# Kernel tuning notes

Hardware: AMD Instinct MI355X
Metric: run time of the kernel (lower is better)

The kernel has to match this reference:

```python
import jax, jax.numpy as jnp
import numpy as np

N_NODES = 100000
N_EDGES = 1600000
F_IN = 256
F_HID = 128
BN_EPS = 1e-3


def setup_inputs() -> dict:
    key = jax.random.key(0)
    ks = jax.random.split(key, 10)
    x = jax.random.normal(ks[0], (N_NODES, F_IN), dtype=jnp.float32)
    edge_index = jax.random.randint(ks[1], (2, N_EDGES), 0, N_NODES, dtype=jnp.int64)
    edge_weight = jax.random.uniform(ks[2], (N_EDGES,), dtype=jnp.float32)
    # Layer 0: GCNConv 256 -> 128, Layer 1: GCNConv 128 -> 128
    W0 = jax.random.normal(ks[3], (F_IN, F_HID), dtype=jnp.float32) * (1.0 / np.sqrt(F_IN))
    b0 = jnp.zeros((F_HID,), dtype=jnp.float32)
    g0 = jnp.ones((F_HID,), dtype=jnp.float32)
    beta0 = jnp.zeros((F_HID,), dtype=jnp.float32)
    W1 = jax.random.normal(ks[4], (F_HID, F_HID), dtype=jnp.float32) * (1.0 / np.sqrt(F_HID))
    b1 = jnp.zeros((F_HID,), dtype=jnp.float32)
    g1 = jnp.ones((F_HID,), dtype=jnp.float32)
    beta1 = jnp.zeros((F_HID,), dtype=jnp.float32)
    return {"x": x, "edge_index": edge_index, "edge_weight": edge_weight,
            "W0": W0, "b0": b0, "g0": g0, "beta0": beta0,
            "W1": W1, "b1": b1, "g1": g1, "beta1": beta1}


def _gcn_conv(x, src, dst, ew, W, b):
    # PyG GCNConv: add self-loops (weight 1), symmetric normalization,
    # linear transform, scatter-aggregate over destination, then bias.
    h = x @ W                                            # [N, F_out]
    deg = jax.ops.segment_sum(ew, dst, num_segments=N_NODES) + 1.0  # +1 self-loop
    dinv = jnp.where(deg > 0, jax.lax.rsqrt(deg), 0.0)   # deg^{-1/2}
    norm = dinv[src] * ew * dinv[dst]                    # [E]
    agg = jax.ops.segment_sum(h[src] * norm[:, None], dst, num_segments=N_NODES)
    agg = agg + (dinv * dinv)[:, None] * h               # self-loop contribution
    return agg + b


def _batchnorm(x, gamma, beta):
    # training-mode BatchNorm1d math (batch stats, biased variance), eps=1e-3
    mu = jnp.mean(x, axis=0)
    var = jnp.mean(jnp.square(x - mu), axis=0)
    return (x - mu) * jax.lax.rsqrt(var + BN_EPS) * gamma + beta


def reference(x, edge_index, edge_weight, W0, b0, g0, beta0, W1, b1, g1, beta1):
    src, dst = edge_index[0], edge_index[1]
    # Layer 0: GCNConv -> BatchNorm -> ReLU -> Dropout(eval=identity)
    h = _gcn_conv(x, src, dst, edge_weight, W0, b0)
    h = jax.nn.relu(_batchnorm(h, g0, beta0))
    # Layer 1
    h = _gcn_conv(h, src, dst, edge_weight, W1, b1)
    h = jax.nn.relu(_batchnorm(h, g1, beta1))
    return h
```

## Files before the change

### kernel.cpp

```cpp
#include <hip/hip_runtime.h>
#include <stdint.h>

#define FIN 256
#define FHID 128
#define BN_EPS 1e-3f

#ifndef USE_GLL
#if defined(__has_builtin)
#if __has_builtin(__builtin_amdgcn_global_load_lds)
#define USE_GLL 1
#else
#define USE_GLL 0
#endif
#else
#define USE_GLL 0
#endif
#endif

typedef short bf16x8 __attribute__((ext_vector_type(8)));
typedef float f32x4 __attribute__((ext_vector_type(4)));

__device__ inline short f2bf(float f) {
    unsigned u = __float_as_uint(f);
    unsigned r = (u + 0x7FFFu + ((u >> 16) & 1u)) >> 16;
    return (short)r;
}
__device__ inline float bflo(unsigned v) { return __uint_as_float(v << 16); }
__device__ inline float bfhi(unsigned v) { return __uint_as_float(v & 0xFFFF0000u); }
__device__ inline float bf2f(short s) {
    return __uint_as_float(((unsigned)(unsigned short)s) << 16);
}

#define DEG_SCALE 131072.0f
#define DEG_INV   (1.0f / 131072.0f)

__global__ __launch_bounds__(256) void k_histprep(const int* __restrict__ ei, int E,
                                                  int HB, int CHUNKH, int nbuk,
                                                  unsigned* __restrict__ bcnt,
                                                  const float* __restrict__ W0,
                                                  const float* __restrict__ W1,
                                                  short* __restrict__ Wt0,
                                                  short* __restrict__ Wt1) {
    __shared__ unsigned hist[1024];
    if ((int)blockIdx.x < HB) {
        for (int i = threadIdx.x; i < nbuk; i += 256) hist[i] = 0;
        __syncthreads();
        const int e0 = blockIdx.x * CHUNKH;
        const int e1 = min(e0 + CHUNKH, E);
        for (int e = e0 + threadIdx.x; e < e1; e += 256)
            atomicAdd(&hist[ei[E + e] >> 7], 1u);
        __syncthreads();
        for (int k = threadIdx.x; k < nbuk; k += 256)
            bcnt[(size_t)blockIdx.x * nbuk + k] = hist[k];
    } else {
        int idx = ((int)blockIdx.x - HB) * 256 + threadIdx.x;
        if (idx < 32768) {
            int n = idx >> 8, k = idx & 255;
            Wt0[idx] = f2bf(W0[k * 128 + n]);
        } else {
            int j = idx - 32768;
            if (j < 16384) {
                int n = j >> 7, k = j & 127;
                Wt1[j] = f2bf(W1[k * 128 + n]);
            }
        }
    }
}

__global__ __launch_bounds__(256) void k_gemm0(const float* __restrict__ X,
                                               const short* __restrict__ Wt,
                                               short* __restrict__ H, int nrows) {
    __shared__ float xs[8192];
    const int t = threadIdx.x;
    const int lane = t & 63;
    const int w = t >> 6;
    const int r0 = blockIdx.x * 32;
    const int l15 = lane & 15;
    const int q = lane >> 4;

#pragma unroll
    for (int i = 0; i < 8; i++) {
        const int row = w * 8 + i;
        int grow = r0 + row; if (grow >= nrows) grow = nrows - 1;
        const char* gsrc = (const char*)(X + (size_t)grow * 256);
        const int swz = (row & 7) << 4;
#if USE_GLL
        __builtin_amdgcn_global_load_lds(gsrc + ((lane * 16) ^ swz),
                                         xs + row * 256, 16, 0, 0);
#else
        const float4 v = *reinterpret_cast<const float4*>(gsrc + ((lane * 16) ^ swz));
        *reinterpret_cast<float4*>((char*)xs + row * 1024 + lane * 16) = v;
#endif
    }
    __syncthreads();

    const int n0 = w * 32;
    const int swzr = (l15 & 7) << 4;

    f32x4 acc[2][2];
#pragma unroll
    for (int mf = 0; mf < 2; mf++)
#pragma unroll
        for (int nf = 0; nf < 2; nf++)
#pragma unroll
            for (int r = 0; r < 4; r++) acc[mf][nf][r] = 0.0f;

#pragma unroll
    for (int ks = 0; ks < 8; ks++) {
        const int cb = ks * 128 + q * 32;
        bf16x8 a[2];
#pragma unroll
        for (int mf = 0; mf < 2; mf++) {
            const char* rb = (const char*)xs + (size_t)(mf * 16 + l15) * 1024;
            const float4 u0 = *reinterpret_cast<const float4*>(rb + (cb ^ swzr));
            const float4 u1 = *reinterpret_cast<const float4*>(rb + ((cb + 16) ^ swzr));
            bf16x8 tt;
            tt[0] = f2bf(u0.x); tt[1] = f2bf(u0.y); tt[2] = f2bf(u0.z); tt[3] = f2bf(u0.w);
            tt[4] = f2bf(u1.x); tt[5] = f2bf(u1.y); tt[6] = f2bf(u1.z); tt[7] = f2bf(u1.w);
            a[mf] = tt;
        }
        const bf16x8 b0 = *reinterpret_cast<const bf16x8*>(
            Wt + (size_t)(n0 + l15) * 256 + ks * 32 + q * 8);
        const bf16x8 b1 = *reinterpret_cast<const bf16x8*>(
            Wt + (size_t)(n0 + 16 + l15) * 256 + ks * 32 + q * 8);
        acc[0][0] = __builtin_amdgcn_mfma_f32_16x16x32_bf16(a[0], b0, acc[0][0], 0, 0, 0);
        acc[1][0] = __builtin_amdgcn_mfma_f32_16x16x32_bf16(a[1], b0, acc[1][0], 0, 0, 0);
        acc[0][1] = __builtin_amdgcn_mfma_f32_16x16x32_bf16(a[0], b1, acc[0][1], 0, 0, 0);
        acc[1][1] = __builtin_amdgcn_mfma_f32_16x16x32_bf16(a[1], b1, acc[1][1], 0, 0, 0);
    }

#pragma unroll
    for (int mf = 0; mf < 2; mf++) {
        const int rbase = r0 + mf * 16 + (lane >> 4) * 4;
#pragma unroll
        for (int r = 0; r < 4; r++) {
            const int row = rbase + r;
            if (row < nrows) {
#pragma unroll
                for (int nf = 0; nf < 2; nf++)
                    H[(size_t)row * 128 + n0 + nf * 16 + l15] = f2bf(acc[mf][nf][r]);
            }
        }
    }
}

__global__ __launch_bounds__(256) void k_gemm1(const short* __restrict__ X,
                                               const short* __restrict__ Wt,
                                               const float* __restrict__ prm,
                                               short* __restrict__ H, int nrows) {
    __shared__ short xs[4096];
    const int t = threadIdx.x;
    const int lane = t & 63;
    const int w = t >> 6;
    const int r0 = blockIdx.x * 32;
    const int l15 = lane & 15;
    const int q = lane >> 4;

#pragma unroll
    for (int j = 0; j < 2; j++) {
        const int rbase = w * 8 + j * 4;
        const int row = rbase + q;
        int grow = r0 + row; if (grow >= nrows) grow = nrows - 1;
        const char* gsrc = (const char*)(X + (size_t)grow * 128);
        const int swz = (row & 7) << 4;
#if USE_GLL
        __builtin_amdgcn_global_load_lds(gsrc + (((lane & 15) * 16) ^ swz),
                                         xs + rbase * 128, 16, 0, 0);
#else
        const uint4 v = *reinterpret_cast<const uint4*>(gsrc + (((lane & 15) * 16) ^ swz));
        *reinterpret_cast<uint4*>((char*)xs + rbase * 256 + lane * 16) = v;
#endif
    }
    __syncthreads();

    const int n0 = w * 32;
    const int swzr = (l15 & 7) << 4;

    f32x4 acc[2][2];
#pragma unroll
    for (int mf = 0; mf < 2; mf++)
#pragma unroll
        for (int nf = 0; nf < 2; nf++)
#pragma unroll
            for (int r = 0; r < 4; r++) acc[mf][nf][r] = 0.0f;

#pragma unroll
    for (int ks = 0; ks < 4; ks++) {
        const int kb = ks * 32 + q * 8;
        const int cb = ks * 64 + q * 16;
        const float4 sc0 = *reinterpret_cast<const float4*>(prm + kb);
        const float4 sc1 = *reinterpret_cast<const float4*>(prm + kb + 4);
        const float4 sh0 = *reinterpret_cast<const float4*>(prm + 128 + kb);
        const float4 sh1 = *reinterpret_cast<const float4*>(prm + 128 + kb + 4);
        bf16x8 a[2];
#pragma unroll
        for (int mf = 0; mf < 2; mf++) {
            const char* rb = (const char*)xs + (size_t)(mf * 16 + l15) * 256;
            const bf16x8 ar = *reinterpret_cast<const bf16x8*>(rb + (cb ^ swzr));
            bf16x8 tt;
            tt[0] = f2bf(fmaxf(bf2f(ar[0]) * sc0.x + sh0.x, 0.f));
            tt[1] = f2bf(fmaxf(bf2f(ar[1]) * sc0.y + sh0.y, 0.f));
            tt[2] = f2bf(fmaxf(bf2f(ar[2]) * sc0.z + sh0.z, 0.f));
            tt[3] = f2bf(fmaxf(bf2f(ar[3]) * sc0.w + sh0.w, 0.f));
            tt[4] = f2bf(fmaxf(bf2f(ar[4]) * sc1.x + sh1.x, 0.f));
            tt[5] = f2bf(fmaxf(bf2f(ar[5]) * sc1.y + sh1.y, 0.f));
            tt[6] = f2bf(fmaxf(bf2f(ar[6]) * sc1.z + sh1.z, 0.f));
            tt[7] = f2bf(fmaxf(bf2f(ar[7]) * sc1.w + sh1.w, 0.f));
            a[mf] = tt;
        }
        const bf16x8 b0 = *reinterpret_cast<const bf16x8*>(
            Wt + (size_t)(n0 + l15) * 128 + kb);
        const bf16x8 b1 = *reinterpret_cast<const bf16x8*>(
            Wt + (size_t)(n0 + 16 + l15) * 128 + kb);
        acc[0][0] = __builtin_amdgcn_mfma_f32_16x16x32_bf16(a[0], b0, acc[0][0], 0, 0, 0);
        acc[1][0] = __builtin_amdgcn_mfma_f32_16x16x32_bf16(a[1], b0, acc[1][0], 0, 0, 0);
        acc[0][1] = __builtin_amdgcn_mfma_f32_16x16x32_bf16(a[0], b1, acc[0][1], 0, 0, 0);
        acc[1][1] = __builtin_amdgcn_mfma_f32_16x16x32_bf16(a[1], b1, acc[1][1], 0, 0, 0);
    }

#pragma unroll
    for (int mf = 0; mf < 2; mf++) {
        const int rbase = r0 + mf * 16 + (lane >> 4) * 4;
#pragma unroll
        for (int r = 0; r < 4; r++) {
            const int row = rbase + r;
            if (row < nrows) {
#pragma unroll
                for (int nf = 0; nf < 2; nf++)
                    H[(size_t)row * 128 + n0 + nf * 16 + l15] = f2bf(acc[mf][nf][r]);
            }
        }
    }
}

__global__ __launch_bounds__(256) void k_phaseB(unsigned* __restrict__ bcnt,
                                                unsigned* __restrict__ btotal,
                                                int HB, int nbuk) {
    __shared__ unsigned lds[256];
    const int k = blockIdx.x;
    const int t = threadIdx.x;
    unsigned v[4];
    unsigned s = 0;
#pragma unroll
    for (int i = 0; i < 4; i++) {
        int j = t * 4 + i;
        v[i] = (j < HB) ? bcnt[(size_t)j * nbuk + k] : 0;
        s += v[i];
    }
    lds[t] = s;
    __syncthreads();
    for (int off = 1; off < 256; off <<= 1) {
        unsigned add = (t >= off) ? lds[t - off] : 0;
        __syncthreads();
        lds[t] += add;
        __syncthreads();
    }
    unsigned run = lds[t] - s;
#pragma unroll
    for (int i = 0; i < 4; i++) {
        int j = t * 4 + i;
        if (j < HB) bcnt[(size_t)j * nbuk + k] = run;
        run += v[i];
    }
    if (t == 255) btotal[k] = lds[255];
}

__global__ __launch_bounds__(256) void k_bsum(const unsigned* __restrict__ btotal,
                                              unsigned* __restrict__ bbase,
                                              int nbuk, int E) {
    __shared__ unsigned lds[256];
    const int t = threadIdx.x;
    unsigned v[4];
    unsigned s = 0;
#pragma unroll
    for (int i = 0; i < 4; i++) {
        int j = t * 4 + i;
        v[i] = (j < nbuk) ? btotal[j] : 0;
        s += v[i];
    }
    lds[t] = s;
    __syncthreads();
    for (int off = 1; off < 256; off <<= 1) {
        unsigned add = (t >= off) ? lds[t - off] : 0;
        __syncthreads();
        lds[t] += add;
        __syncthreads();
    }
    unsigned run = lds[t] - s;
#pragma unroll
    for (int i = 0; i < 4; i++) {
        int j = t * 4 + i;
        if (j < nbuk) bbase[j] = run;
        run += v[i];
    }
    if (t == 255) bbase[nbuk] = (unsigned)E;
}

__global__ __launch_bounds__(256) void k_phaseC(const int* __restrict__ ei,
                                                const float* __restrict__ ew,
                                                int E, int CHUNKC, int nbuk, int sub,
                                                const unsigned* __restrict__ bcnt,
                                                const unsigned* __restrict__ bbase,
                                                int2* __restrict__ recs_mid) {
    __shared__ unsigned curs[1024];
    const int b = blockIdx.x;
    for (int k = threadIdx.x; k < nbuk; k += 256)
        curs[k] = bbase[k] + bcnt[(size_t)(b * sub) * nbuk + k];
    __syncthreads();
    const int e0 = b * CHUNKC;
    const int e1 = min(e0 + CHUNKC, E);
    for (int e = e0 + threadIdx.x; e < e1; e += 256) {
        int src = ei[e];
        int dst = ei[E + e];
        unsigned pos = atomicAdd(&curs[dst >> 7], 1u);
        recs_mid[pos] = make_int2(src | ((dst & 127) << 17), __float_as_int(ew[e]));
    }
}

__global__ __launch_bounds__(256) void k_phaseD(const int2* __restrict__ recs_mid,
                                                const unsigned* __restrict__ bbase,
                                                float* __restrict__ dinv,
                                                int* __restrict__ rowptr,
                                                int2* __restrict__ recs,
                                                int n, int E) {
    __shared__ unsigned cnt[128], wsum[128], rank[128], sc[128], base[128];
    __shared__ float dloc[128];
    const int k = blockIdx.x;
    const int t = threadIdx.x;
    if (t < 128) { cnt[t] = 0; wsum[t] = 0; rank[t] = 0; }
    __syncthreads();
    const unsigned s0 = bbase[k], s1 = bbase[k + 1];
    for (unsigned i = s0 + t; i < s1; i += 256) {
        int2 r = recs_mid[i];
        int dl = (r.x >> 17) & 127;
        atomicAdd(&cnt[dl], 1u);
        atomicAdd(&wsum[dl], (unsigned)(__int_as_float(r.y) * DEG_SCALE));
    }
    __syncthreads();
    if (t < 128) sc[t] = cnt[t];
    __syncthreads();
    for (int off = 1; off < 128; off <<= 1) {
        unsigned add = (t < 128 && t >= off) ? sc[t - off] : 0;
        __syncthreads();
        if (t < 128) sc[t] += add;
        __syncthreads();
    }
    if (t < 128) {
        unsigned excl = sc[t] - cnt[t];
        base[t] = s0 + excl;
        int dst = k * 128 + t;
        if (dst < n) {
            float deg = (float)wsum[t] * DEG_INV + 1.0f;
            float dv = rsqrtf(deg);
            dloc[t] = dv;
            dinv[dst] = dv;
            rowptr[dst] = (int)(s0 + excl);
        }
    }
    if (k == 0 && t == 0) rowptr[n] = E;
    __syncthreads();
    for (unsigned i = s0 + t; i < s1; i += 256) {
        int2 r = recs_mid[i];
        int dl = (r.x >> 17) & 127;
        unsigned rr = atomicAdd(&rank[dl], 1u);
        float w2 = __int_as_float(r.y) * dloc[dl];
        recs[base[dl] + rr] = make_int2(r.x & 0x1FFFF, __float_as_int(w2));
    }
}

__global__ __launch_bounds__(256) void k_phaseE(int2* __restrict__ recs,
                                                const float* __restrict__ dinv, int E) {
    int i = blockIdx.x * 256 + threadIdx.x;
    if (i < E) {
        int2 r = recs[i];
        float w = __int_as_float(r.y) * dinv[r.x];
        recs[i] = make_int2(r.x, __float_as_int(w));
    }
}

__global__ __launch_bounds__(256) void k_gather_stats(const short* __restrict__ h,
                                                      short* __restrict__ aggbf,
                                                      const int* __restrict__ rowptr,
                                                      const int2* __restrict__ recs,
                                                      const float* __restrict__ dinv,
                                                      const float* __restrict__ bias,
                                                      float* __restrict__ partial,
                                                      int n, int nstreams) {
    __shared__ float lsum[4][128], lsq[4][128];
    const int w = threadIdx.x >> 6;
    const int lane = threadIdx.x & 63;
    const int q3 = lane >> 4;
    const int f8 = (lane & 15) * 8;
    const float4 bv0 = *reinterpret_cast<const float4*>(bias + f8);
    const float4 bv1 = *reinterpret_cast<const float4*>(bias + f8 + 4);
    float s[8], qq[8];
#pragma unroll
    for (int j = 0; j < 8; j++) { s[j] = 0.f; qq[j] = 0.f; }

    for (int node = blockIdx.x * 16 + w * 4 + q3; node < n; node += nstreams) {
        float a[8];
#pragma unroll
        for (int j = 0; j < 8; j++) a[j] = 0.f;
        int e = rowptr[node];
        const int end = rowptr[node + 1];
        for (; e + 4 <= end; e += 4) {
            const int2 r0 = recs[e];
            const int2 r1 = recs[e + 1];
            const int2 r2 = recs[e + 2];
            const int2 r3 = recs[e + 3];
            const uint4 v0 = *reinterpret_cast<const uint4*>(h + (size_t)r0.x * 128 + f8);
            const uint4 v1 = *reinterpret_cast<const uint4*>(h + (size_t)r1.x * 128 + f8);
            const uint4 v2 = *reinterpret_cast<const uint4*>(h + (size_t)r2.x * 128 + f8);
            const uint4 v3 = *reinterpret_cast<const uint4*>(h + (size_t)r3.x * 128 + f8);
            const float w0 = __int_as_float(r0.y);
            const float w1 = __int_as_float(r1.y);
            const float w2 = __int_as_float(r2.y);
            const float w3 = __int_as_float(r3.y);
            a[0] += bflo(v0.x) * w0; a[1] += bfhi(v0.x) * w0;
            a[2] += bflo(v0.y) * w0; a[3] += bfhi(v0.y) * w0;
            a[4] += bflo(v0.z) * w0; a[5] += bfhi(v0.z) * w0;
            a[6] += bflo(v0.w) * w0; a[7] += bfhi(v0.w) * w0;
            a[0] += bflo(v1.x) * w1; a[1] += bfhi(v1.x) * w1;
            a[2] += bflo(v1.y) * w1; a[3] += bfhi(v1.y) * w1;
            a[4] += bflo(v1.z) * w1; a[5] += bfhi(v1.z) * w1;
            a[6] += bflo(v1.w) * w1; a[7] += bfhi(v1.w) * w1;
            a[0] += bflo(v2.x) * w2; a[1] += bfhi(v2.x) * w2;
            a[2] += bflo(v2.y) * w2; a[3] += bfhi(v2.y) * w2;
            a[4] += bflo(v2.z) * w2; a[5] += bfhi(v2.z) * w2;
            a[6] += bflo(v2.w) * w2; a[7] += bfhi(v2.w) * w2;
            a[0] += bflo(v3.x) * w3; a[1] += bfhi(v3.x) * w3;
            a[2] += bflo(v3.y) * w3; a[3] += bfhi(v3.y) * w3;
            a[4] += bflo(v3.z) * w3; a[5] += bfhi(v3.z) * w3;
            a[6] += bflo(v3.w) * w3; a[7] += bfhi(v3.w) * w3;
        }
        for (; e < end; e++) {
            const int2 r = recs[e];
            const uint4 v = *reinterpret_cast<const uint4*>(h + (size_t)r.x * 128 + f8);
            const float w0 = __int_as_float(r.y);
            a[0] += bflo(v.x) * w0; a[1] += bfhi(v.x) * w0;
            a[2] += bflo(v.y) * w0; a[3] += bfhi(v.y) * w0;
            a[4] += bflo(v.z) * w0; a[5] += bfhi(v.z) * w0;
            a[6] += bflo(v.w) * w0; a[7] += bfhi(v.w) * w0;
        }
        const float di = dinv[node];
        const float sl = di * di;
        const uint4 hv = *reinterpret_cast<const uint4*>(h + (size_t)node * 128 + f8);
        float o[8];
        o[0] = a[0] + bflo(hv.x) * sl + bv0.x;
        o[1] = a[1] + bfhi(hv.x) * sl + bv0.y;
        o[2] = a[2] + bflo(hv.y) * sl + bv0.z;
        o[3] = a[3] + bfhi(hv.y) * sl + bv0.w;
        o[4] = a[4] + bflo(hv.z) * sl + bv1.x;
        o[5] = a[5] + bfhi(hv.z) * sl + bv1.y;
        o[6] = a[6] + bflo(hv.w) * sl + bv1.z;
        o[7] = a[7] + bfhi(hv.w) * sl + bv1.w;
        bf16x8 ob;
#pragma unroll
        for (int j = 0; j < 8; j++) ob[j] = f2bf(o[j]);
        *reinterpret_cast<bf16x8*>(aggbf + (size_t)node * 128 + f8) = ob;
#pragma unroll
        for (int j = 0; j < 8; j++) { s[j] += o[j]; qq[j] += o[j] * o[j]; }
    }

#pragma unroll
    for (int j = 0; j < 8; j++) {
        s[j] += __shfl_xor(s[j], 16);  s[j] += __shfl_xor(s[j], 32);
        qq[j] += __shfl_xor(qq[j], 16); qq[j] += __shfl_xor(qq[j], 32);
    }
    if (q3 == 0) {
        *reinterpret_cast<float4*>(&lsum[w][f8]) = make_float4(s[0], s[1], s[2], s[3]);
        *reinterpret_cast<float4*>(&lsum[w][f8 + 4]) = make_float4(s[4], s[5], s[6], s[7]);
        *reinterpret_cast<float4*>(&lsq[w][f8]) = make_float4(qq[0], qq[1], qq[2], qq[3]);
        *reinterpret_cast<float4*>(&lsq[w][f8 + 4]) = make_float4(qq[4], qq[5], qq[6], qq[7]);
    }
    __syncthreads();
    const int t = threadIdx.x;
    if (t < 128) {
        float ps = lsum[0][t] + lsum[1][t] + lsum[2][t] + lsum[3][t];
        float pq = lsq[0][t] + lsq[1][t] + lsq[2][t] + lsq[3][t];
        partial[(size_t)blockIdx.x * 256 + t] = ps;
        partial[(size_t)blockIdx.x * 256 + 128 + t] = pq;
    }
}

__global__ __launch_bounds__(256) void k_stats_bn(const float* __restrict__ partial,
                                                  const float* __restrict__ g,
                                                  const float* __restrict__ beta,
                                                  float* __restrict__ prm,
                                                  int nblk, int n) {
    __shared__ float wsm[4], wqm[4];
    const int f = blockIdx.x;
    const int t = threadIdx.x;
    const int per = nblk / 256;
    float s = 0.f, q = 0.f;
    for (int i = 0; i < per; i++) {
        int p = t * per + i;
        s += partial[(size_t)p * 256 + f];
        q += partial[(size_t)p * 256 + 128 + f];
    }
#pragma unroll
    for (int off = 1; off < 64; off <<= 1) {
        s += __shfl_xor(s, off);
        q += __shfl_xor(q, off);
    }
    if ((t & 63) == 0) { wsm[t >> 6] = s; wqm[t >> 6] = q; }
    __syncthreads();
    if (t == 0) {
        float S = wsm[0] + wsm[1] + wsm[2] + wsm[3];
        float Q = wqm[0] + wqm[1] + wqm[2] + wqm[3];
        float inv_n = 1.0f / (float)n;
        float mu = S * inv_n;
        float var = Q * inv_n - mu * mu;
        float sc = rsqrtf(var + BN_EPS) * g[f];
        prm[f] = sc;
        prm[128 + f] = beta[f] - mu * sc;
    }
}

__global__ __launch_bounds__(256) void k_bn_relu(const short* __restrict__ xbf,
                                                 float* __restrict__ y,
                                                 const float* __restrict__ prm, int n) {
    int idx = blockIdx.x * blockDim.x + threadIdx.x;
    const int total = n * 16;
    for (; idx < total; idx += gridDim.x * blockDim.x) {
        int node = idx >> 4;
        int f8 = (idx & 15) * 8;
        const uint4 v = *reinterpret_cast<const uint4*>(xbf + (size_t)node * 128 + f8);
        const float4 sc0 = *reinterpret_cast<const float4*>(prm + f8);
        const float4 sc1 = *reinterpret_cast<const float4*>(prm + f8 + 4);
        const float4 sh0 = *reinterpret_cast<const float4*>(prm + 128 + f8);
        const float4 sh1 = *reinterpret_cast<const float4*>(prm + 128 + f8 + 4);
        float4 o0, o1;
        o0.x = fmaxf(bflo(v.x) * sc0.x + sh0.x, 0.f);
        o0.y = fmaxf(bfhi(v.x) * sc0.y + sh0.y, 0.f);
        o0.z = fmaxf(bflo(v.y) * sc0.z + sh0.z, 0.f);
        o0.w = fmaxf(bfhi(v.y) * sc0.w + sh0.w, 0.f);
        o1.x = fmaxf(bflo(v.z) * sc1.x + sh1.x, 0.f);
        o1.y = fmaxf(bfhi(v.z) * sc1.y + sh1.y, 0.f);
        o1.z = fmaxf(bflo(v.w) * sc1.z + sh1.z, 0.f);
        o1.w = fmaxf(bfhi(v.w) * sc1.w + sh1.w, 0.f);
        float* yp = y + (size_t)node * 128 + f8;
        *reinterpret_cast<float4*>(yp) = o0;
        *reinterpret_cast<float4*>(yp + 4) = o1;
    }
}

extern "C" void kernel_launch(void* const* d_in, const int* in_sizes, int n_in,
                              void* d_out, int out_size, void* d_ws, size_t ws_size,
                              hipStream_t stream) {
    const float* x   = (const float*)d_in[0];
    const int*   ei  = (const int*)d_in[1];
    const float* ew  = (const float*)d_in[2];
    const float* W0  = (const float*)d_in[3];
    const float* b0  = (const float*)d_in[4];
    const float* g0  = (const float*)d_in[5];
    const float* be0 = (const float*)d_in[6];
    const float* W1  = (const float*)d_in[7];
    const float* b1  = (const float*)d_in[8];
    const float* g1  = (const float*)d_in[9];
    const float* be1 = (const float*)d_in[10];
    float* out = (float*)d_out;

    const int N = in_sizes[0] / FIN;
    const int E = in_sizes[2];
    const int NBUK = (N + 127) >> 7;
    const int HB = 1024;
    const int CHUNKH = (E + HB - 1) / HB;
    const int CBC = 256;
    const int SUB = HB / CBC;
    const int CHUNKC = CHUNKH * SUB;
    const int GB = 2048;

    short* aggbf    = (short*)d_ws;
    short* hbf      = aggbf + (size_t)N * 128;
    int2*  recs     = (int2*)(hbf + (size_t)N * 128);
    int2*  recs_mid = recs + E;
    unsigned* bcnt  = (unsigned*)(recs_mid + E);
    unsigned* btotal= bcnt + (size_t)HB * NBUK;
    unsigned* bbase = btotal + NBUK;
    float* dinv     = (float*)(bbase + NBUK + 1);
    int*   rowptr   = (int*)(dinv + N);
    float* prm      = (float*)(rowptr + N + 1);
    float* partial  = prm + 256;

    short* Wt0 = (short*)d_out;
    short* Wt1 = Wt0 + 256 * 128;

    const int gemm_blocks = (N + 31) / 32;

    k_histprep<<<HB + 192, 256, 0, stream>>>(ei, E, HB, CHUNKH, NBUK, bcnt,
                                             W0, W1, Wt0, Wt1);
    k_gemm0<<<gemm_blocks, 256, 0, stream>>>(x, Wt0, hbf, N);

    k_phaseB<<<NBUK, 256, 0, stream>>>(bcnt, btotal, HB, NBUK);
    k_bsum<<<1, 256, 0, stream>>>(btotal, bbase, NBUK, E);
    k_phaseC<<<CBC, 256, 0, stream>>>(ei, ew, E, CHUNKC, NBUK, SUB, bcnt, bbase, recs_mid);
    k_phaseD<<<NBUK, 256, 0, stream>>>(recs_mid, bbase, dinv, rowptr, recs, N, E);
    k_phaseE<<<(E + 255) / 256, 256, 0, stream>>>(recs, dinv, E);

    k_gather_stats<<<GB, 256, 0, stream>>>(hbf, aggbf, rowptr, recs, dinv, b0,
                                           partial, N, GB * 16);
    k_stats_bn<<<128, 256, 0, stream>>>(partial, g0, be0, prm, GB, N);

    k_gemm1<<<gemm_blocks, 256, 0, stream>>>(aggbf, Wt1, prm, hbf, N);
    k_gather_stats<<<GB, 256, 0, stream>>>(hbf, aggbf, rowptr, recs, dinv, b1,
                                           partial, N, GB * 16);
    k_stats_bn<<<128, 256, 0, stream>>>(partial, g1, be1, prm, GB, N);
    k_bn_relu<<<2048, 256, 0, stream>>>(aggbf, out, prm, N);
}
```

Measured before the change: 321.7 us.

## Sort nodes by degree for gather load balance and fold source dinv into gather

Per-node in-degree counts are recorded in phaseD, then a three-kernel counting sort (histogram, scan, scatter) builds a degree-sorted node permutation. The gather kernel processes nodes in that order, so the four nodes sharing a wavefront have similar edge counts and less lane divergence. The separate phaseE pass that multiplied edge weights by source dinv is removed; the gather now loads dinv[src] per edge instead, in both layers. This adds three small launches and extra random reads per edge, and the permuted order scatters output writes.

```diff
diff --git a/kernel.cpp b/kernel.cpp
--- a/kernel.cpp
+++ b/kernel.cpp
@@ -321,6 +321,7 @@
                                                 const unsigned* __restrict__ bbase,
                                                 float* __restrict__ dinv,
                                                 int* __restrict__ rowptr,
+                                                int* __restrict__ deg,
                                                 int2* __restrict__ recs,
                                                 int n, int E) {
     __shared__ unsigned cnt[128], wsum[128], rank[128], sc[128], base[128];
@@ -350,11 +351,12 @@
         base[t] = s0 + excl;
         int dst = k * 128 + t;
         if (dst < n) {
-            float deg = (float)wsum[t] * DEG_INV + 1.0f;
-            float dv = rsqrtf(deg);
+            float dg = (float)wsum[t] * DEG_INV + 1.0f;
+            float dv = rsqrtf(dg);
             dloc[t] = dv;
             dinv[dst] = dv;
             rowptr[dst] = (int)(s0 + excl);
+            deg[dst] = min((int)cnt[t], 63);
         }
     }
     if (k == 0 && t == 0) rowptr[n] = E;
@@ -368,13 +370,57 @@
     }
 }
 
-__global__ __launch_bounds__(256) void k_phaseE(int2* __restrict__ recs,
-                                                const float* __restrict__ dinv, int E) {
-    int i = blockIdx.x * 256 + threadIdx.x;
-    if (i < E) {
-        int2 r = recs[i];
-        float w = __int_as_float(r.y) * dinv[r.x];
-        recs[i] = make_int2(r.x, __float_as_int(w));
+__global__ __launch_bounds__(256) void k_sorthist(const int* __restrict__ deg,
+                                                  unsigned* __restrict__ shist,
+                                                  int n, int SB, int CH) {
+    __shared__ unsigned h[64];
+    if (threadIdx.x < 64) h[threadIdx.x] = 0;
+    __syncthreads();
+    const int e0 = blockIdx.x * CH;
+    const int e1 = min(e0 + CH, n);
+    for (int i = e0 + threadIdx.x; i < e1; i += 256)
+        atomicAdd(&h[deg[i]], 1u);
+    __syncthreads();
+    if (threadIdx.x < 64)
+        shist[(size_t)threadIdx.x * SB + blockIdx.x] = h[threadIdx.x];
+}
+
+__global__ __launch_bounds__(256) void k_sortscan(unsigned* __restrict__ shist,
+                                                  int total) {
+    __shared__ unsigned lds[256];
+    const int t = threadIdx.x;
+    const int per = total / 256;
+    unsigned s = 0;
+    for (int i = 0; i < per; i++) s += shist[t * per + i];
+    lds[t] = s;
+    __syncthreads();
+    for (int off = 1; off < 256; off <<= 1) {
+        unsigned add = (t >= off) ? lds[t - off] : 0;
+        __syncthreads();
+        lds[t] += add;
+        __syncthreads();
+    }
+    unsigned run = lds[t] - s;
+    for (int i = 0; i < per; i++) {
+        unsigned v = shist[t * per + i];
+        shist[t * per + i] = run;
+        run += v;
+    }
+}
+
+__global__ __launch_bounds__(256) void k_sortscatter(const int* __restrict__ deg,
+                                                     const unsigned* __restrict__ shist,
+                                                     int* __restrict__ perm,
+                                                     int n, int SB, int CH) {
+    __shared__ unsigned curs[64];
+    if (threadIdx.x < 64)
+        curs[threadIdx.x] = shist[(size_t)threadIdx.x * SB + blockIdx.x];
+    __syncthreads();
+    const int e0 = blockIdx.x * CH;
+    const int e1 = min(e0 + CH, n);
+    for (int i = e0 + threadIdx.x; i < e1; i += 256) {
+        unsigned p = atomicAdd(&curs[deg[i]], 1u);
+        perm[p] = i;
     }
 }
 
@@ -383,6 +429,7 @@
                                                       const int* __restrict__ rowptr,
                                                       const int2* __restrict__ recs,
                                                       const float* __restrict__ dinv,
+                                                      const int* __restrict__ perm,
                                                       const float* __restrict__ bias,
                                                       float* __restrict__ partial,
                                                       int n, int nstreams) {
@@ -397,7 +444,8 @@
 #pragma unroll
     for (int j = 0; j < 8; j++) { s[j] = 0.f; qq[j] = 0.f; }
 
-    for (int node = blockIdx.x * 16 + w * 4 + q3; node < n; node += nstreams) {
+    for (int pidx = blockIdx.x * 16 + w * 4 + q3; pidx < n; pidx += nstreams) {
+        const int node = perm[pidx];
         float a[8];
 #pragma unroll
         for (int j = 0; j < 8; j++) a[j] = 0.f;
@@ -408,14 +456,18 @@
             const int2 r1 = recs[e + 1];
             const int2 r2 = recs[e + 2];
             const int2 r3 = recs[e + 3];
+            const float d0 = dinv[r0.x];
+            const float d1 = dinv[r1.x];
+            const float d2 = dinv[r2.x];
+            const float d3 = dinv[r3.x];
             const uint4 v0 = *reinterpret_cast<const uint4*>(h + (size_t)r0.x * 128 + f8);
             const uint4 v1 = *reinterpret_cast<const uint4*>(h + (size_t)r1.x * 128 + f8);
             const uint4 v2 = *reinterpret_cast<const uint4*>(h + (size_t)r2.x * 128 + f8);
             const uint4 v3 = *reinterpret_cast<const uint4*>(h + (size_t)r3.x * 128 + f8);
-            const float w0 = __int_as_float(r0.y);
-            const float w1 = __int_as_float(r1.y);
-            const float w2 = __int_as_float(r2.y);
-            const float w3 = __int_as_float(r3.y);
+            const float w0 = __int_as_float(r0.y) * d0;
+            const float w1 = __int_as_float(r1.y) * d1;
+            const float w2 = __int_as_float(r2.y) * d2;
+            const float w3 = __int_as_float(r3.y) * d3;
             a[0] += bflo(v0.x) * w0; a[1] += bfhi(v0.x) * w0;
             a[2] += bflo(v0.y) * w0; a[3] += bfhi(v0.y) * w0;
             a[4] += bflo(v0.z) * w0; a[5] += bfhi(v0.z) * w0;
@@ -435,8 +487,9 @@
         }
         for (; e < end; e++) {
             const int2 r = recs[e];
+            const float d = dinv[r.x];
             const uint4 v = *reinterpret_cast<const uint4*>(h + (size_t)r.x * 128 + f8);
-            const float w0 = __int_as_float(r.y);
+            const float w0 = __int_as_float(r.y) * d;
             a[0] += bflo(v.x) * w0; a[1] += bfhi(v.x) * w0;
             a[2] += bflo(v.y) * w0; a[3] += bfhi(v.y) * w0;
             a[4] += bflo(v.z) * w0; a[5] += bfhi(v.z) * w0;
@@ -569,6 +622,8 @@
     const int CBC = 256;
     const int SUB = HB / CBC;
     const int CHUNKC = CHUNKH * SUB;
+    const int SB = 256;
+    const int CHS = (N + SB - 1) / SB;
     const int GB = 2048;
 
     short* aggbf    = (short*)d_ws;
@@ -580,7 +635,10 @@
     unsigned* bbase = btotal + NBUK;
     float* dinv     = (float*)(bbase + NBUK + 1);
     int*   rowptr   = (int*)(dinv + N);
-    float* prm      = (float*)(rowptr + N + 1);
+    int*   deg      = rowptr + N + 1;
+    int*   perm     = deg + N;
+    unsigned* shist = (unsigned*)(perm + N);
+    float* prm      = (float*)(shist + 64 * SB);
     float* partial  = prm + 256;
 
     short* Wt0 = (short*)d_out;
@@ -595,15 +653,17 @@
     k_phaseB<<<NBUK, 256, 0, stream>>>(bcnt, btotal, HB, NBUK);
     k_bsum<<<1, 256, 0, stream>>>(btotal, bbase, NBUK, E);
     k_phaseC<<<CBC, 256, 0, stream>>>(ei, ew, E, CHUNKC, NBUK, SUB, bcnt, bbase, recs_mid);
-    k_phaseD<<<NBUK, 256, 0, stream>>>(recs_mid, bbase, dinv, rowptr, recs, N, E);
-    k_phaseE<<<(E + 255) / 256, 256, 0, stream>>>(recs, dinv, E);
-
-    k_gather_stats<<<GB, 256, 0, stream>>>(hbf, aggbf, rowptr, recs, dinv, b0,
+    k_phaseD<<<NBUK, 256, 0, stream>>>(recs_mid, bbase, dinv, rowptr, deg, recs, N, E);
+    k_sorthist<<<SB, 256, 0, stream>>>(deg, shist, N, SB, CHS);
+    k_sortscan<<<1, 256, 0, stream>>>(shist, 64 * SB);
+    k_sortscatter<<<SB, 256, 0, stream>>>(deg, shist, perm, N, SB, CHS);
+
+    k_gather_stats<<<GB, 256, 0, stream>>>(hbf, aggbf, rowptr, recs, dinv, perm, b0,
                                            partial, N, GB * 16);
     k_stats_bn<<<128, 256, 0, stream>>>(partial, g0, be0, prm, GB, N);
 
     k_gemm1<<<gemm_blocks, 256, 0, stream>>>(aggbf, Wt1, prm, hbf, N);
-    k_gather_stats<<<GB, 256, 0, stream>>>(hbf, aggbf, rowptr, recs, dinv, b1,
+    k_gather_stats<<<GB, 256, 0, stream>>>(hbf, aggbf, rowptr, recs, dinv, perm, b1,
                                            partial, N, GB * 16);
     k_stats_bn<<<128, 256, 0, stream>>>(partial, g1, be1, prm, GB, N);
     k_bn_relu<<<2048, 256, 0, stream>>>(aggbf, out, prm, N);
```

Result: slower. 342.3 us (+6.4%).

## Fuse scatter phase with GEMM0 and fold source dinv into gather

Applied to the files above, without the earlier changes.

Merges the edge-scatter phase and the first GEMM into a single launch, splitting the grid by block index so the memory-bound scatter and the MFMA GEMM run concurrently. The scatter loop now reads edge indices and weights as int4/float4 vectors. The separate pass that scaled each edge weight by dinv[src] is removed, and that factor is instead looked up and multiplied inside both gather kernels. This drops one launch and a full read-write pass over the edge records, at the cost of an extra random dinv load per edge in each of the two gathers.

```diff
diff --git a/kernel.cpp b/kernel.cpp
--- a/kernel.cpp
+++ b/kernel.cpp
@@ -67,14 +67,14 @@
     }
 }
 
-__global__ __launch_bounds__(256) void k_gemm0(const float* __restrict__ X,
-                                               const short* __restrict__ Wt,
-                                               short* __restrict__ H, int nrows) {
-    __shared__ float xs[8192];
+__device__ __forceinline__ void gemm0_body(int bid, float* xs,
+                                           const float* __restrict__ X,
+                                           const short* __restrict__ Wt,
+                                           short* __restrict__ H, int nrows) {
     const int t = threadIdx.x;
     const int lane = t & 63;
     const int w = t >> 6;
-    const int r0 = blockIdx.x * 32;
+    const int r0 = bid * 32;
     const int l15 = lane & 15;
     const int q = lane >> 4;
 
@@ -141,6 +141,58 @@
                     H[(size_t)row * 128 + n0 + nf * 16 + l15] = f2bf(acc[mf][nf][r]);
             }
         }
+    }
+}
+
+__global__ __launch_bounds__(256) void k_phaseCG(const int* __restrict__ ei,
+                                                 const float* __restrict__ ew,
+                                                 int E, int CHUNKC, int nbuk, int sub,
+                                                 const unsigned* __restrict__ bcnt,
+                                                 const unsigned* __restrict__ bbase,
+                                                 int2* __restrict__ recs_mid,
+                                                 int CBC,
+                                                 const float* __restrict__ X,
+                                                 const short* __restrict__ Wt,
+                                                 short* __restrict__ H, int nrows) {
+    __shared__ float xs[8192];
+    if ((int)blockIdx.x < CBC) {
+        unsigned* curs = (unsigned*)xs;
+        const int b = blockIdx.x;
+        for (int k = threadIdx.x; k < nbuk; k += 256)
+            curs[k] = bbase[k] + bcnt[(size_t)(b * sub) * nbuk + k];
+        __syncthreads();
+        const int e0 = b * CHUNKC;
+        const int e1 = min(e0 + CHUNKC, E);
+        for (int base = e0; base < e1; base += 1024) {
+            const int e = base + threadIdx.x * 4;
+            if (e + 3 < e1) {
+                const int4 s4 = *reinterpret_cast<const int4*>(ei + e);
+                const int4 d4 = *reinterpret_cast<const int4*>(ei + E + e);
+                const float4 w4 = *reinterpret_cast<const float4*>(ew + e);
+                unsigned p0 = atomicAdd(&curs[d4.x >> 7], 1u);
+                recs_mid[p0] = make_int2(s4.x | ((d4.x & 127) << 17), __float_as_int(w4.x));
+                unsigned p1 = atomicAdd(&curs[d4.y >> 7], 1u);
+                recs_mid[p1] = make_int2(s4.y | ((d4.y & 127) << 17), __float_as_int(w4.y));
+                unsigned p2 = atomicAdd(&curs[d4.z >> 7], 1u);
+                recs_mid[p2] = make_int2(s4.z | ((d4.z & 127) << 17), __float_as_int(w4.z));
+                unsigned p3 = atomicAdd(&curs[d4.w >> 7], 1u);
+                recs_mid[p3] = make_int2(s4.w | ((d4.w & 127) << 17), __float_as_int(w4.w));
+            } else {
+#pragma unroll
+                for (int j = 0; j < 4; j++) {
+                    const int ee = e + j;
+                    if (ee < e1) {
+                        int src = ei[ee];
+                        int dst = ei[E + ee];
+                        unsigned pos = atomicAdd(&curs[dst >> 7], 1u);
+                        recs_mid[pos] = make_int2(src | ((dst & 127) << 17),
+                                                  __float_as_int(ew[ee]));
+                    }
+                }
+            }
+        }
+    } else {
+        gemm0_body((int)blockIdx.x - CBC, xs, X, Wt, H, nrows);
     }
 }
 
@@ -296,27 +348,6 @@
     if (t == 255) bbase[nbuk] = (unsigned)E;
 }
 
-__global__ __launch_bounds__(256) void k_phaseC(const int* __restrict__ ei,
-                                                const float* __restrict__ ew,
-                                                int E, int CHUNKC, int nbuk, int sub,
-                                                const unsigned* __restrict__ bcnt,
-                                                const unsigned* __restrict__ bbase,
-                                                int2* __restrict__ recs_mid) {
-    __shared__ unsigned curs[1024];
-    const int b = blockIdx.x;
-    for (int k = threadIdx.x; k < nbuk; k += 256)
-        curs[k] = bbase[k] + bcnt[(size_t)(b * sub) * nbuk + k];
-    __syncthreads();
-    const int e0 = b * CHUNKC;
-    const int e1 = min(e0 + CHUNKC, E);
-    for (int e = e0 + threadIdx.x; e < e1; e += 256) {
-        int src = ei[e];
-        int dst = ei[E + e];
-        unsigned pos = atomicAdd(&curs[dst >> 7], 1u);
-        recs_mid[pos] = make_int2(src | ((dst & 127) << 17), __float_as_int(ew[e]));
-    }
-}
-
 __global__ __launch_bounds__(256) void k_phaseD(const int2* __restrict__ recs_mid,
                                                 const unsigned* __restrict__ bbase,
                                                 float* __restrict__ dinv,
@@ -350,8 +381,8 @@
         base[t] = s0 + excl;
         int dst = k * 128 + t;
         if (dst < n) {
-            float deg = (float)wsum[t] * DEG_INV + 1.0f;
-            float dv = rsqrtf(deg);
+            float dg = (float)wsum[t] * DEG_INV + 1.0f;
+            float dv = rsqrtf(dg);
             dloc[t] = dv;
             dinv[dst] = dv;
             rowptr[dst] = (int)(s0 + excl);
@@ -365,16 +396,6 @@
         unsigned rr = atomicAdd(&rank[dl], 1u);
         float w2 = __int_as_float(r.y) * dloc[dl];
         recs[base[dl] + rr] = make_int2(r.x & 0x1FFFF, __float_as_int(w2));
-    }
-}
-
-__global__ __launch_bounds__(256) void k_phaseE(int2* __restrict__ recs,
-                                                const float* __restrict__ dinv, int E) {
-    int i = blockIdx.x * 256 + threadIdx.x;
-    if (i < E) {
-        int2 r = recs[i];
-        float w = __int_as_float(r.y) * dinv[r.x];
-        recs[i] = make_int2(r.x, __float_as_int(w));
     }
 }
 
@@ -408,14 +429,18 @@
             const int2 r1 = recs[e + 1];
             const int2 r2 = recs[e + 2];
             const int2 r3 = recs[e + 3];
+            const float d0 = dinv[r0.x];
+            const float d1 = dinv[r1.x];
+            const float d2 = dinv[r2.x];
+            const float d3 = dinv[r3.x];
             const uint4 v0 = *reinterpret_cast<const uint4*>(h + (size_t)r0.x * 128 + f8);
             const uint4 v1 = *reinterpret_cast<const uint4*>(h + (size_t)r1.x * 128 + f8);
             const uint4 v2 = *reinterpret_cast<const uint4*>(h + (size_t)r2.x * 128 + f8);
             const uint4 v3 = *reinterpret_cast<const uint4*>(h + (size_t)r3.x * 128 + f8);
-            const float w0 = __int_as_float(r0.y);
-            const float w1 = __int_as_float(r1.y);
-            const float w2 = __int_as_float(r2.y);
-            const float w3 = __int_as_float(r3.y);
+            const float w0 = __int_as_float(r0.y) * d0;
+            const float w1 = __int_as_float(r1.y) * d1;
+            const float w2 = __int_as_float(r2.y) * d2;
+            const float w3 = __int_as_float(r3.y) * d3;
             a[0] += bflo(v0.x) * w0; a[1] += bfhi(v0.x) * w0;
             a[2] += bflo(v0.y) * w0; a[3] += bfhi(v0.y) * w0;
             a[4] += bflo(v0.z) * w0; a[5] += bfhi(v0.z) * w0;
@@ -435,8 +460,9 @@
         }
         for (; e < end; e++) {
             const int2 r = recs[e];
+            const float d = dinv[r.x];
             const uint4 v = *reinterpret_cast<const uint4*>(h + (size_t)r.x * 128 + f8);
-            const float w0 = __int_as_float(r.y);
+            const float w0 = __int_as_float(r.y) * d;
             a[0] += bflo(v.x) * w0; a[1] += bfhi(v.x) * w0;
             a[2] += bflo(v.y) * w0; a[3] += bfhi(v.y) * w0;
             a[4] += bflo(v.z) * w0; a[5] += bfhi(v.z) * w0;
@@ -590,13 +616,13 @@
 
     k_histprep<<<HB + 192, 256, 0, stream>>>(ei, E, HB, CHUNKH, NBUK, bcnt,
                                              W0, W1, Wt0, Wt1);
-    k_gemm0<<<gemm_blocks, 256, 0, stream>>>(x, Wt0, hbf, N);
-
     k_phaseB<<<NBUK, 256, 0, stream>>>(bcnt, btotal, HB, NBUK);
     k_bsum<<<1, 256, 0, stream>>>(btotal, bbase, NBUK, E);
-    k_phaseC<<<CBC, 256, 0, stream>>>(ei, ew, E, CHUNKC, NBUK, SUB, bcnt, bbase, recs_mid);
+
+    k_phaseCG<<<CBC + gemm_blocks, 256, 0, stream>>>(ei, ew, E, CHUNKC, NBUK, SUB,
+                                                     bcnt, bbase, recs_mid, CBC,
+                                                     x, Wt0, hbf, N);
     k_phaseD<<<NBUK, 256, 0, stream>>>(recs_mid, bbase, dinv, rowptr, recs, N, E);
-    k_phaseE<<<(E + 255) / 256, 256, 0, stream>>>(recs, dinv, E);
 
     k_gather_stats<<<GB, 256, 0, stream>>>(hbf, aggbf, rowptr, recs, dinv, b0,
                                            partial, N, GB * 16);
```

After: 289.6 us, median of 2. -10.0%, faster.
